# Kernel optimization log

Measured on AMD Instinct MI355X. Metric: run time of the kernel, lower is better.

## Reference

```python
import jax, jax.numpy as jnp
import numpy as np

VOCAB = 21128
D_WENLAN = 2048
SENT_LEN = 44  # hard-coded in original forward


def setup_inputs() -> dict:
    key = jax.random.key(0)
    ks = jax.random.split(key, 8)
    B, S, P = 32, 8, 32
    L = S * SENT_LEN  # 352
    concat_output = jax.random.normal(ks[0], (B, S, D_WENLAN), jnp.float32)
    input_ids = jax.random.randint(ks[1], (B, L), 0, VOCAB, jnp.int32)
    topic_ids = jax.random.randint(ks[2], (B, P), 0, VOCAB, jnp.int32)
    tpw_att_mask = jnp.ones((B, P), jnp.int32)
    tpw_type_ids = jnp.zeros((B, P), jnp.int32)
    attention_mask = jnp.ones((B, L), jnp.int32)
    type_ids = jax.random.randint(ks[3], (B, L), 0, 8, jnp.int32)
    token_table = jax.random.normal(ks[4], (VOCAB, D_WENLAN), jnp.float32) * 0.02
    W1 = jax.random.normal(ks[5], (D_WENLAN, 512), jnp.float32) * 0.02
    b1 = jnp.zeros((512,), jnp.float32)
    W2 = jax.random.normal(ks[6], (512, 768), jnp.float32) * 0.02
    b2 = jnp.zeros((768,), jnp.float32)
    return dict(concat_output=concat_output, input_ids=input_ids, topic_ids=topic_ids,
                tpw_att_mask=tpw_att_mask, tpw_type_ids=tpw_type_ids,
                attention_mask=attention_mask, type_ids=type_ids,
                token_table=token_table, W1=W1, b1=b1, W2=W2, b2=b2)


def reference(concat_output, input_ids, topic_ids, tpw_att_mask, tpw_type_ids,
              attention_mask, type_ids, token_table, W1, b1, W2, b2):
    B, S, D = concat_output.shape
    # vectorized replacement of the python double-loop dict lookups:
    topic_emb = token_table[topic_ids]                      # [B,P,2048]
    inp_emb = token_table[input_ids]                        # [B,L,2048]
    # scatter-add: each sentence block of 44 tokens gets its concat_output row added
    inp_emb = inp_emb.reshape(B, S, SENT_LEN, D) + concat_output[:, :, None, :]
    input_embs = jnp.concatenate([topic_emb, inp_emb.reshape(B, S * SENT_LEN, D)], axis=1)
    # projector MLP (Linear -> tanh -> Linear)
    h = jnp.tanh(jnp.einsum('btd,dk->btk', input_embs, W1) + b1)
    gpt_input_embs = jnp.einsum('btk,ke->bte', h, W2) + b2   # [B,P+L,768]
    # auxiliary concatenated tensors fed to gpt2 (is_train=True path)
    labels = jnp.concatenate([topic_ids, input_ids], axis=1)
    full_type_ids = jnp.concatenate([tpw_type_ids, type_ids], axis=1)
    full_att_mask = jnp.concatenate([tpw_att_mask, attention_mask], axis=1)
    return gpt_input_embs, labels, full_type_ids, full_att_mask
```

## Files before the change

### kernel.cpp

```cpp
#include <hip/hip_runtime.h>
#include <math.h>

typedef _Float16 half8 __attribute__((ext_vector_type(8)));
typedef float f32x4 __attribute__((ext_vector_type(4)));

#define BB 32
#define SS 8
#define PP 32
#define SENT 44
#define LL 352
#define TT 384
#define DD 2048
#define H1 512
#define H2 768
#define MM (BB*TT)
#define OUT0 (MM*H2)

#define GLL16(g, l) __builtin_amdgcn_global_load_lds( \
    (const __attribute__((address_space(1))) void*)(g), \
    (__attribute__((address_space(3))) void*)(l), 16, 0, 0)

__global__ __launch_bounds__(256) void transpose_f16_kernel(
    const float* __restrict__ src, _Float16* __restrict__ dst, int R, int C)
{
    __shared__ float tile[32][33];
    int c0 = blockIdx.x * 32;
    int r0 = blockIdx.y * 32;
    int tx = threadIdx.x & 31;
    int ty = threadIdx.x >> 5;
    #pragma unroll
    for (int i = 0; i < 4; ++i)
        tile[ty + i*8][tx] = src[(size_t)(r0 + ty + i*8) * C + c0 + tx];
    __syncthreads();
    #pragma unroll
    for (int i = 0; i < 4; ++i)
        dst[(size_t)(c0 + ty + i*8) * R + r0 + tx] = (_Float16)tile[tx][ty + i*8];
}

__global__ __launch_bounds__(256) void gemm1_kernel(
    const float*    __restrict__ token_table,
    const int*      __restrict__ topic_ids,
    const int*      __restrict__ input_ids,
    const float*    __restrict__ concat_output,
    const _Float16* __restrict__ W1T,
    const float*    __restrict__ b1,
    _Float16*       __restrict__ Hout)
{
    const int tid  = threadIdx.x;
    const int wid  = tid >> 6;
    const int lane = tid & 63;

    const int logical = ((blockIdx.x & 7) * 48) + (blockIdx.x >> 3);
    const int bm = logical >> 1;
    const int bn = logical & 1;

    __shared__ _Float16 As[2][64 * 64];
    __shared__ _Float16 Bs[2][256 * 64];

    const int arow = tid >> 2;
    const int akq  = (tid & 3) * 16;
    const int aswz = (arow & 7) << 3;

    {
    }
    const int m = bm * 64 + arow;
    const int b = m / TT;
    const int t = m % TT;
    const float* aptr;
    const float* addp = nullptr;
    if (t < PP) {
        aptr = token_table + (size_t)topic_ids[b * PP + t] * DD;
    } else {
        int u = t - PP;
        aptr = token_table + (size_t)input_ids[b * LL + u] * DD;
        addp = concat_output + ((size_t)b * SS + (u / SENT)) * DD;
    }

    const int rl = lane >> 3;
    const int cg = lane & 7;
    const _Float16* bsrc = W1T + (size_t)(bn * 256 + wid * 64 + rl) * DD
                               + ((cg ^ rl) << 3);

    #define G1B(buf, k0) {                                                 \
        _Pragma("unroll")                                                  \
        for (int q = 0; q < 8; ++q)                                        \
            GLL16(bsrc + (size_t)q * 8 * DD + (k0),                        \
                  &Bs[buf][(wid * 8 + q) * 512]);                          \
    }

    #define LOADA(S, k0) {                                                 \
        const float* ap = aptr + (k0) + akq;                               \
        float4 v0 = *(const float4*)(ap);                                  \
        float4 v1 = *(const float4*)(ap + 4);                              \
        float4 v2 = *(const float4*)(ap + 8);                              \
        float4 v3 = *(const float4*)(ap + 12);                             \
        if (addp) {                                                        \
            const float* cp = addp + (k0) + akq;                           \
            float4 c0 = *(const float4*)(cp);                              \
            float4 c1 = *(const float4*)(cp + 4);                          \
            float4 c2 = *(const float4*)(cp + 8);                          \
            float4 c3 = *(const float4*)(cp + 12);                         \
            v0.x += c0.x; v0.y += c0.y; v0.z += c0.z; v0.w += c0.w;        \
            v1.x += c1.x; v1.y += c1.y; v1.z += c1.z; v1.w += c1.w;        \
            v2.x += c2.x; v2.y += c2.y; v2.z += c2.z; v2.w += c2.w;        \
            v3.x += c3.x; v3.y += c3.y; v3.z += c3.z; v3.w += c3.w;        \
        }                                                                  \
        S[0]=v0.x; S[1]=v0.y; S[2]=v0.z; S[3]=v0.w;                        \
        S[4]=v1.x; S[5]=v1.y; S[6]=v1.z; S[7]=v1.w;                        \
        S[8]=v2.x; S[9]=v2.y; S[10]=v2.z; S[11]=v2.w;                      \
        S[12]=v3.x; S[13]=v3.y; S[14]=v3.z; S[15]=v3.w;                    \
    }

    #define WRITEA(S, buf) {                                               \
        half8 h0, h1;                                                      \
        _Pragma("unroll")                                                  \
        for (int j = 0; j < 8; ++j) { h0[j] = (_Float16)S[j];              \
                                      h1[j] = (_Float16)S[8 + j]; }        \
        *(half8*)&As[buf][(arow * 64 + akq) ^ aswz]     = h0;              \
        *(half8*)&As[buf][(arow * 64 + akq + 8) ^ aswz] = h1;              \
    }

    const int wrow = (wid >> 1) * 32;
    const int wcol = (wid & 1) * 128;
    const int fr   = lane & 15;
    const int fg   = lane >> 4;

    f32x4 acc[2][8] = {};

    #define MFMAP(buf) {                                                   \
        _Pragma("unroll")                                                  \
        for (int kk = 0; kk < 2; ++kk) {                                   \
            half8 af[2], bf[8];                                            \
            _Pragma("unroll")                                              \
            for (int i = 0; i < 2; ++i) {                                  \
                int row = wrow + i * 16 + fr;                              \
                af[i] = *(const half8*)&As[buf][                           \
                    (row * 64 + kk * 32 + fg * 8) ^ ((row & 7) << 3)];     \
            }                                                              \
            _Pragma("unroll")                                              \
            for (int j = 0; j < 8; ++j) {                                  \
                int row = wcol + j * 16 + fr;                              \
                bf[j] = *(const half8*)&Bs[buf][                           \
                    (row * 64 + kk * 32 + fg * 8) ^ ((row & 7) << 3)];     \
            }                                                              \
            _Pragma("unroll")                                              \
            for (int i = 0; i < 2; ++i)                                    \
                _Pragma("unroll")                                          \
                for (int j = 0; j < 8; ++j)                                \
                    acc[i][j] = __builtin_amdgcn_mfma_f32_16x16x32_f16(    \
                        af[i], bf[j], acc[i][j], 0, 0, 0);                 \
        }                                                                  \
    }

    float a0[16], a1[16];

    G1B(0, 0);
    LOADA(a0, 0);
    LOADA(a1, 64);
    WRITEA(a0, 0);
    __syncthreads();

    for (int tt = 0; tt < 16; ++tt) {
        const int t2 = tt * 2;
        G1B(1, (t2 + 1) * 64);
        if (t2 + 2 < 32) LOADA(a0, (t2 + 2) * 64);
        MFMAP(0);
        WRITEA(a1, 1);
        __syncthreads();
        if (t2 + 2 < 32) G1B(0, (t2 + 2) * 64);
        if (t2 + 3 < 32) LOADA(a1, (t2 + 3) * 64);
        MFMAP(1);
        if (t2 + 2 < 32) WRITEA(a0, 0);
        __syncthreads();
    }

    #pragma unroll
    for (int i = 0; i < 2; ++i) {
        #pragma unroll
        for (int j = 0; j < 8; ++j) {
            int col = bn * 256 + wcol + j * 16 + fr;
            float bias = b1[col];
            #pragma unroll
            for (int r = 0; r < 4; ++r) {
                int row = bm * 64 + wrow + i * 16 + fg * 4 + r;
                Hout[(size_t)row * H1 + col] = (_Float16)tanhf(acc[i][j][r] + bias);
            }
        }
    }
    #undef G1B
    #undef LOADA
    #undef WRITEA
    #undef MFMAP
}

__global__ __launch_bounds__(256) void gemm2_kernel(
    const _Float16* __restrict__ Hin,
    const _Float16* __restrict__ W2T,
    const float*    __restrict__ b2,
    float*          __restrict__ out)
{
    const int tid  = threadIdx.x;
    const int wid  = tid >> 6;
    const int lane = tid & 63;

    const int logical = ((blockIdx.x & 7) * 72) + (blockIdx.x >> 3);
    const int bm = logical / 6;
    const int bn = logical % 6;

    __shared__ _Float16 As[2][128 * 64];
    __shared__ _Float16 Bs[2][128 * 64];

    const int rl = lane >> 3;
    const int cg = lane & 7;
    const _Float16* asrc = Hin + (size_t)(bm * 128 + wid * 32 + rl) * H1
                               + ((cg ^ rl) << 3);
    const _Float16* bsrc = W2T + (size_t)(bn * 128 + wid * 32 + rl) * H1
                               + ((cg ^ rl) << 3);

    #define G2_ISSUE(buf, k0) {                                            \
        _Pragma("unroll")                                                  \
        for (int q = 0; q < 4; ++q) {                                      \
            GLL16(asrc + (size_t)q * 8 * H1 + (k0),                        \
                  &As[buf][(wid * 4 + q) * 512]);                          \
            GLL16(bsrc + (size_t)q * 8 * H1 + (k0),                        \
                  &Bs[buf][(wid * 4 + q) * 512]);                          \
        }                                                                  \
    }

    const int wrow = (wid >> 1) * 64;
    const int wcol = (wid & 1) * 64;
    const int fr   = lane & 15;
    const int fg   = lane >> 4;

    f32x4 acc[4][4] = {};

    G2_ISSUE(0, 0);

    const int NT = H1 / 64;
    for (int t = 0; t < NT; ++t) {
        __syncthreads();
        if (t + 1 < NT) G2_ISSUE((t + 1) & 1, (t + 1) * 64);
        const int cb = t & 1;
        #pragma unroll
        for (int kk = 0; kk < 2; ++kk) {
            half8 af[4], bf[4];
            #pragma unroll
            for (int i = 0; i < 4; ++i) {
                int row = wrow + i * 16 + fr;
                af[i] = *(const half8*)&As[cb][
                    (row * 64 + kk * 32 + fg * 8) ^ ((row & 7) << 3)];
            }
            #pragma unroll
            for (int j = 0; j < 4; ++j) {
                int row = wcol + j * 16 + fr;
                bf[j] = *(const half8*)&Bs[cb][
                    (row * 64 + kk * 32 + fg * 8) ^ ((row & 7) << 3)];
            }
            #pragma unroll
            for (int i = 0; i < 4; ++i)
                #pragma unroll
                for (int j = 0; j < 4; ++j)
                    acc[i][j] = __builtin_amdgcn_mfma_f32_16x16x32_f16(af[i], bf[j], acc[i][j], 0, 0, 0);
        }
    }

    #pragma unroll
    for (int i = 0; i < 4; ++i) {
        #pragma unroll
        for (int j = 0; j < 4; ++j) {
            int col = bn * 128 + wcol + j * 16 + fr;
            float bias = b2[col];
            #pragma unroll
            for (int r = 0; r < 4; ++r) {
                int row = bm * 128 + wrow + i * 16 + fg * 4 + r;
                out[(size_t)row * H2 + col] = acc[i][j][r] + bias;
            }
        }
    }
    #undef G2_ISSUE
}

__global__ __launch_bounds__(256) void aux_kernel(
    const int* __restrict__ topic_ids,
    const int* __restrict__ input_ids,
    const int* __restrict__ tpw_type_ids,
    const int* __restrict__ type_ids,
    const int* __restrict__ tpw_att_mask,
    const int* __restrict__ attention_mask,
    float* __restrict__ out)
{
    int idx = blockIdx.x * 256 + threadIdx.x;
    if (idx >= MM) return;
    int b = idx / TT, t = idx % TT;
    int lab, ty, mk;
    if (t < PP) {
        lab = topic_ids[b * PP + t];
        ty  = tpw_type_ids[b * PP + t];
        mk  = tpw_att_mask[b * PP + t];
    } else {
        int u = t - PP;
        lab = input_ids[b * LL + u];
        ty  = type_ids[b * LL + u];
        mk  = attention_mask[b * LL + u];
    }
    out[OUT0 + idx]          = (float)lab;
    out[OUT0 + MM + idx]     = (float)ty;
    out[OUT0 + 2 * MM + idx] = (float)mk;
}

extern "C" void kernel_launch(void* const* d_in, const int* in_sizes, int n_in,
                              void* d_out, int out_size, void* d_ws, size_t ws_size,
                              hipStream_t stream) {
    const float* concat_output  = (const float*)d_in[0];
    const int*   input_ids      = (const int*)d_in[1];
    const int*   topic_ids      = (const int*)d_in[2];
    const int*   tpw_att_mask   = (const int*)d_in[3];
    const int*   tpw_type_ids   = (const int*)d_in[4];
    const int*   attention_mask = (const int*)d_in[5];
    const int*   type_ids       = (const int*)d_in[6];
    const float* token_table    = (const float*)d_in[7];
    const float* W1             = (const float*)d_in[8];
    const float* b1             = (const float*)d_in[9];
    const float* W2             = (const float*)d_in[10];
    const float* b2             = (const float*)d_in[11];
    float* out = (float*)d_out;

    _Float16* w1t = (_Float16*)d_ws;
    _Float16* w2t = w1t + (size_t)H1 * DD;
    _Float16* Hws = w2t + (size_t)H2 * H1;

    transpose_f16_kernel<<<dim3(H1 / 32, DD / 32), 256, 0, stream>>>(W1, w1t, DD, H1);
    transpose_f16_kernel<<<dim3(H2 / 32, H1 / 32), 256, 0, stream>>>(W2, w2t, H1, H2);
    aux_kernel<<<(MM + 255) / 256, 256, 0, stream>>>(
        topic_ids, input_ids, tpw_type_ids, type_ids, tpw_att_mask, attention_mask, out);

    gemm1_kernel<<<(MM / 64) * (H1 / 256), 256, 0, stream>>>(
        token_table, topic_ids, input_ids, concat_output, w1t, b1, Hws);
    gemm2_kernel<<<(MM / 128) * (H2 / 128), 256, 0, stream>>>(Hws, w2t, b2, out);
}
```

Baseline: 104.3 us.

## Precompute concat_output projection separately and retile both GEMMs

```diff
diff --git a/kernel.cpp b/kernel.cpp
--- a/kernel.cpp
+++ b/kernel.cpp
@@ -37,160 +37,245 @@
         dst[(size_t)(c0 + ty + i*8) * R + r0 + tx] = (_Float16)tile[tx][ty + i*8];
 }
 
+#define LOADA_T(S, ap, k0) {                                               \
+    const float* _p = (ap) + (k0) + akq;                                   \
+    float4 v0 = *(const float4*)(_p);                                      \
+    float4 v1 = *(const float4*)(_p + 4);                                  \
+    float4 v2 = *(const float4*)(_p + 8);                                  \
+    float4 v3 = *(const float4*)(_p + 12);                                 \
+    S[0]=v0.x; S[1]=v0.y; S[2]=v0.z; S[3]=v0.w;                            \
+    S[4]=v1.x; S[5]=v1.y; S[6]=v1.z; S[7]=v1.w;                            \
+    S[8]=v2.x; S[9]=v2.y; S[10]=v2.z; S[11]=v2.w;                          \
+    S[12]=v3.x; S[13]=v3.y; S[14]=v3.z; S[15]=v3.w;                        \
+}
+
+#define WRITEA_T(S, dst) {                                                 \
+    half8 h0, h1;                                                          \
+    _Pragma("unroll")                                                      \
+    for (int _j = 0; _j < 8; ++_j) { h0[_j] = (_Float16)S[_j];             \
+                                     h1[_j] = (_Float16)S[8 + _j]; }       \
+    *(half8*)&dst[(arow * 64 + akq) ^ aswz]     = h0;                      \
+    *(half8*)&dst[(arow * 64 + akq + 8) ^ aswz] = h1;                      \
+}
+
+__global__ __launch_bounds__(256) void c1_kernel(
+    const float*    __restrict__ concat_output,
+    const _Float16* __restrict__ W1T,
+    float*          __restrict__ C1)
+{
+    const int tid  = threadIdx.x;
+    const int wid  = tid >> 6;
+    const int lane = tid & 63;
+    const int bm = blockIdx.x >> 2;
+    const int bn = blockIdx.x & 3;
+
+    __shared__ _Float16 As[2][64 * 64];
+    __shared__ _Float16 Bs[2][128 * 64];
+
+    const int arow = tid >> 2;
+    const int akq  = (tid & 3) * 16;
+    const int aswz = (arow & 7) << 3;
+    const float* aptr = concat_output + (size_t)(bm * 64 + arow) * DD;
+
+    const int rl = lane >> 3;
+    const int cg = lane & 7;
+    const _Float16* bsrc = W1T + (size_t)(bn * 128 + wid * 32 + rl) * DD
+                               + ((cg ^ rl) << 3);
+
+    #define C1B(buf, k0) {                                                \
+        _Pragma("unroll")                                                 \
+        for (int q = 0; q < 4; ++q)                                       \
+            GLL16(bsrc + (size_t)q * 8 * DD + (k0),                       \
+                  &Bs[buf][(wid * 4 + q) * 512]);                         \
+    }
+
+    const int wrow = (wid >> 1) * 32;
+    const int wcol = (wid & 1) * 64;
+    const int fr   = lane & 15;
+    const int fg   = lane >> 4;
+
+    f32x4 acc[2][4] = {};
+    float a0[16], a1[16];
+
+    C1B(0, 0);
+    LOADA_T(a0, aptr, 0);
+    LOADA_T(a1, aptr, 64);
+    WRITEA_T(a0, As[0]);
+    __syncthreads();
+
+    #define C1_MFMA(buf) {                                                \
+        _Pragma("unroll")                                                 \
+        for (int kk = 0; kk < 2; ++kk) {                                  \
+            half8 af[2], bf[4];                                           \
+            _Pragma("unroll")                                             \
+            for (int i = 0; i < 2; ++i) {                                 \
+                int row = wrow + i * 16 + fr;                             \
+                af[i] = *(const half8*)&As[buf][                          \
+                    (row * 64 + kk * 32 + fg * 8) ^ ((row & 7) << 3)];    \
+            }                                                             \
+            _Pragma("unroll")                                             \
+            for (int j = 0; j < 4; ++j) {                                 \
+                int row = wcol + j * 16 + fr;                             \
+                bf[j] = *(const half8*)&Bs[buf][                          \
+                    (row * 64 + kk * 32 + fg * 8) ^ ((row & 7) << 3)];    \
+            }                                                             \
+            _Pragma("unroll")                                             \
+            for (int i = 0; i < 2; ++i)                                   \
+                _Pragma("unroll")                                         \
+                for (int j = 0; j < 4; ++j)                               \
+                    acc[i][j] = __builtin_amdgcn_mfma_f32_16x16x32_f16(   \
+                        af[i], bf[j], acc[i][j], 0, 0, 0);                \
+        }                                                                 \
+    }
+
+    for (int tt = 0; tt < 16; ++tt) {
+        const int t2 = tt * 2;
+        C1B(1, (t2 + 1) * 64);
+        if (t2 + 2 < 32) LOADA_T(a0, aptr, (t2 + 2) * 64);
+        C1_MFMA(0);
+        WRITEA_T(a1, As[1]);
+        __syncthreads();
+        if (t2 + 2 < 32) C1B(0, (t2 + 2) * 64);
+        if (t2 + 3 < 32) LOADA_T(a1, aptr, (t2 + 3) * 64);
+        C1_MFMA(1);
+        if (t2 + 2 < 32) WRITEA_T(a0, As[0]);
+        __syncthreads();
+    }
+
+    #pragma unroll
+    for (int i = 0; i < 2; ++i)
+        #pragma unroll
+        for (int j = 0; j < 4; ++j) {
+            int col = bn * 128 + wcol + j * 16 + fr;
+            #pragma unroll
+            for (int r = 0; r < 4; ++r) {
+                int row = bm * 64 + wrow + i * 16 + fg * 4 + r;
+                C1[(size_t)row * H1 + col] = acc[i][j][r];
+            }
+        }
+    #undef C1B
+    #undef C1_MFMA
+}
+
 __global__ __launch_bounds__(256) void gemm1_kernel(
     const float*    __restrict__ token_table,
     const int*      __restrict__ topic_ids,
     const int*      __restrict__ input_ids,
-    const float*    __restrict__ concat_output,
     const _Float16* __restrict__ W1T,
     const float*    __restrict__ b1,
+    const float*    __restrict__ C1,
     _Float16*       __restrict__ Hout)
 {
     const int tid  = threadIdx.x;
     const int wid  = tid >> 6;
     const int lane = tid & 63;
 
-    const int logical = ((blockIdx.x & 7) * 48) + (blockIdx.x >> 3);
-    const int bm = logical >> 1;
-    const int bn = logical & 1;
+    const int logical = ((blockIdx.x & 7) * 96) + (blockIdx.x >> 3);
+    const int bm = logical >> 2;
+    const int bn = logical & 3;
 
     __shared__ _Float16 As[2][64 * 64];
-    __shared__ _Float16 Bs[2][256 * 64];
+    __shared__ _Float16 Bs[2][128 * 64];
 
     const int arow = tid >> 2;
     const int akq  = (tid & 3) * 16;
     const int aswz = (arow & 7) << 3;
 
-    {
-    }
     const int m = bm * 64 + arow;
     const int b = m / TT;
     const int t = m % TT;
     const float* aptr;
-    const float* addp = nullptr;
     if (t < PP) {
         aptr = token_table + (size_t)topic_ids[b * PP + t] * DD;
     } else {
-        int u = t - PP;
-        aptr = token_table + (size_t)input_ids[b * LL + u] * DD;
-        addp = concat_output + ((size_t)b * SS + (u / SENT)) * DD;
+        aptr = token_table + (size_t)input_ids[b * LL + (t - PP)] * DD;
     }
 
     const int rl = lane >> 3;
     const int cg = lane & 7;
-    const _Float16* bsrc = W1T + (size_t)(bn * 256 + wid * 64 + rl) * DD
+    const _Float16* bsrc = W1T + (size_t)(bn * 128 + wid * 32 + rl) * DD
                                + ((cg ^ rl) << 3);
 
-    #define G1B(buf, k0) {                                                 \
-        _Pragma("unroll")                                                  \
-        for (int q = 0; q < 8; ++q)                                        \
-            GLL16(bsrc + (size_t)q * 8 * DD + (k0),                        \
-                  &Bs[buf][(wid * 8 + q) * 512]);                          \
-    }
-
-    #define LOADA(S, k0) {                                                 \
-        const float* ap = aptr + (k0) + akq;                               \
-        float4 v0 = *(const float4*)(ap);                                  \
-        float4 v1 = *(const float4*)(ap + 4);                              \
-        float4 v2 = *(const float4*)(ap + 8);                              \
-        float4 v3 = *(const float4*)(ap + 12);                             \
-        if (addp) {                                                        \
-            const float* cp = addp + (k0) + akq;                           \
-            float4 c0 = *(const float4*)(cp);                              \
-            float4 c1 = *(const float4*)(cp + 4);                          \
-            float4 c2 = *(const float4*)(cp + 8);                          \
-            float4 c3 = *(const float4*)(cp + 12);                         \
-            v0.x += c0.x; v0.y += c0.y; v0.z += c0.z; v0.w += c0.w;        \
-            v1.x += c1.x; v1.y += c1.y; v1.z += c1.z; v1.w += c1.w;        \
-            v2.x += c2.x; v2.y += c2.y; v2.z += c2.z; v2.w += c2.w;        \
-            v3.x += c3.x; v3.y += c3.y; v3.z += c3.z; v3.w += c3.w;        \
-        }                                                                  \
-        S[0]=v0.x; S[1]=v0.y; S[2]=v0.z; S[3]=v0.w;                        \
-        S[4]=v1.x; S[5]=v1.y; S[6]=v1.z; S[7]=v1.w;                        \
-        S[8]=v2.x; S[9]=v2.y; S[10]=v2.z; S[11]=v2.w;                      \
-        S[12]=v3.x; S[13]=v3.y; S[14]=v3.z; S[15]=v3.w;                    \
-    }
-
-    #define WRITEA(S, buf) {                                               \
-        half8 h0, h1;                                                      \
-        _Pragma("unroll")                                                  \
-        for (int j = 0; j < 8; ++j) { h0[j] = (_Float16)S[j];              \
-                                      h1[j] = (_Float16)S[8 + j]; }        \
-        *(half8*)&As[buf][(arow * 64 + akq) ^ aswz]     = h0;              \
-        *(half8*)&As[buf][(arow * 64 + akq + 8) ^ aswz] = h1;              \
+    #define G1B(buf, k0) {                                                \
+        _Pragma("unroll")                                                 \
+        for (int q = 0; q < 4; ++q)                                       \
+            GLL16(bsrc + (size_t)q * 8 * DD + (k0),                       \
+                  &Bs[buf][(wid * 4 + q) * 512]);                         \
     }
 
     const int wrow = (wid >> 1) * 32;
-    const int wcol = (wid & 1) * 128;
+    const int wcol = (wid & 1) * 64;
     const int fr   = lane & 15;
     const int fg   = lane >> 4;
 
-    f32x4 acc[2][8] = {};
-
-    #define MFMAP(buf) {                                                   \
-        _Pragma("unroll")                                                  \
-        for (int kk = 0; kk < 2; ++kk) {                                   \
-            half8 af[2], bf[8];                                            \
-            _Pragma("unroll")                                              \
-            for (int i = 0; i < 2; ++i) {                                  \
-                int row = wrow + i * 16 + fr;                              \
-                af[i] = *(const half8*)&As[buf][                           \
-                    (row * 64 + kk * 32 + fg * 8) ^ ((row & 7) << 3)];     \
-            }                                                              \
-            _Pragma("unroll")                                              \
-            for (int j = 0; j < 8; ++j) {                                  \
-                int row = wcol + j * 16 + fr;                              \
-                bf[j] = *(const half8*)&Bs[buf][                           \
-                    (row * 64 + kk * 32 + fg * 8) ^ ((row & 7) << 3)];     \
-            }                                                              \
-            _Pragma("unroll")                                              \
-            for (int i = 0; i < 2; ++i)                                    \
-                _Pragma("unroll")                                          \
-                for (int j = 0; j < 8; ++j)                                \
-                    acc[i][j] = __builtin_amdgcn_mfma_f32_16x16x32_f16(    \
-                        af[i], bf[j], acc[i][j], 0, 0, 0);                 \
-        }                                                                  \
-    }
-
+    f32x4 acc[2][4] = {};
     float a0[16], a1[16];
 
     G1B(0, 0);
-    LOADA(a0, 0);
-    LOADA(a1, 64);
-    WRITEA(a0, 0);
+    LOADA_T(a0, aptr, 0);
+    LOADA_T(a1, aptr, 64);
+    WRITEA_T(a0, As[0]);
     __syncthreads();
+
+    #define G1_MFMA(buf) {                                                \
+        _Pragma("unroll")                                                 \
+        for (int kk = 0; kk < 2; ++kk) {                                  \
+            half8 af[2], bf[4];                                           \
+            _Pragma("unroll")                                             \
+            for (int i = 0; i < 2; ++i) {                                 \
+                int row = wrow + i * 16 + fr;                             \
+                af[i] = *(const half8*)&As[buf][                          \
+                    (row * 64 + kk * 32 + fg * 8) ^ ((row & 7) << 3)];    \
+            }                                                             \
+            _Pragma("unroll")                                             \
+            for (int j = 0; j < 4; ++j) {                                 \
+                int row = wcol + j * 16 + fr;                             \
+                bf[j] = *(const half8*)&Bs[buf][                          \
+                    (row * 64 + kk * 32 + fg * 8) ^ ((row & 7) << 3)];    \
+            }                                                             \
+            _Pragma("unroll")                                             \
+            for (int i = 0; i < 2; ++i)                                   \
+                _Pragma("unroll")                                         \
+                for (int j = 0; j < 4; ++j)                               \
+                    acc[i][j] = __builtin_amdgcn_mfma_f32_16x16x32_f16(   \
+                        af[i], bf[j], acc[i][j], 0, 0, 0);                \
+        }                                                                 \
+    }
 
     for (int tt = 0; tt < 16; ++tt) {
         const int t2 = tt * 2;
         G1B(1, (t2 + 1) * 64);
-        if (t2 + 2 < 32) LOADA(a0, (t2 + 2) * 64);
-        MFMAP(0);
-        WRITEA(a1, 1);
+        if (t2 + 2 < 32) LOADA_T(a0, aptr, (t2 + 2) * 64);
+        G1_MFMA(0);
+        WRITEA_T(a1, As[1]);
         __syncthreads();
         if (t2 + 2 < 32) G1B(0, (t2 + 2) * 64);
-        if (t2 + 3 < 32) LOADA(a1, (t2 + 3) * 64);
-        MFMAP(1);
-        if (t2 + 2 < 32) WRITEA(a0, 0);
+        if (t2 + 3 < 32) LOADA_T(a1, aptr, (t2 + 3) * 64);
+        G1_MFMA(1);
+        if (t2 + 2 < 32) WRITEA_T(a0, As[0]);
         __syncthreads();
     }
 
     #pragma unroll
     for (int i = 0; i < 2; ++i) {
         #pragma unroll
-        for (int j = 0; j < 8; ++j) {
-            int col = bn * 256 + wcol + j * 16 + fr;
+        for (int j = 0; j < 4; ++j) {
+            int col = bn * 128 + wcol + j * 16 + fr;
             float bias = b1[col];
             #pragma unroll
             for (int r = 0; r < 4; ++r) {
                 int row = bm * 64 + wrow + i * 16 + fg * 4 + r;
-                Hout[(size_t)row * H1 + col] = (_Float16)tanhf(acc[i][j][r] + bias);
+                int rb = row / TT;
+                int rt = row - rb * TT;
+                float v = acc[i][j][r] + bias;
+                if (rt >= PP)
+                    v += C1[(size_t)(rb * SS + (rt - PP) / SENT) * H1 + col];
+                Hout[(size_t)row * H1 + col] = (_Float16)tanhf(v);
             }
         }
     }
     #undef G1B
-    #undef LOADA
-    #undef WRITEA
-    #undef MFMAP
+    #undef G1_MFMA
 }
 
 __global__ __launch_bounds__(256) void gemm2_kernel(
@@ -203,36 +288,37 @@
     const int wid  = tid >> 6;
     const int lane = tid & 63;
 
-    const int logical = ((blockIdx.x & 7) * 72) + (blockIdx.x >> 3);
-    const int bm = logical / 6;
-    const int bn = logical % 6;
-
-    __shared__ _Float16 As[2][128 * 64];
-    __shared__ _Float16 Bs[2][128 * 64];
+    const int logical = ((blockIdx.x & 7) * 64) + (blockIdx.x >> 3);
+    const int bm = logical >> 2;
+    const int bn = logical & 3;
+
+    __shared__ _Float16 As[2][96 * 64];
+    __shared__ _Float16 Bs[2][192 * 64];
 
     const int rl = lane >> 3;
     const int cg = lane & 7;
-    const _Float16* asrc = Hin + (size_t)(bm * 128 + wid * 32 + rl) * H1
+    const _Float16* asrc = Hin + (size_t)(bm * 96 + wid * 24 + rl) * H1
                                + ((cg ^ rl) << 3);
-    const _Float16* bsrc = W2T + (size_t)(bn * 128 + wid * 32 + rl) * H1
+    const _Float16* bsrc = W2T + (size_t)(bn * 192 + wid * 48 + rl) * H1
                                + ((cg ^ rl) << 3);
 
-    #define G2_ISSUE(buf, k0) {                                            \
-        _Pragma("unroll")                                                  \
-        for (int q = 0; q < 4; ++q) {                                      \
-            GLL16(asrc + (size_t)q * 8 * H1 + (k0),                        \
-                  &As[buf][(wid * 4 + q) * 512]);                          \
-            GLL16(bsrc + (size_t)q * 8 * H1 + (k0),                        \
-                  &Bs[buf][(wid * 4 + q) * 512]);                          \
-        }                                                                  \
-    }
-
-    const int wrow = (wid >> 1) * 64;
-    const int wcol = (wid & 1) * 64;
+    #define G2_ISSUE(buf, k0) {                                           \
+        _Pragma("unroll")                                                 \
+        for (int q = 0; q < 3; ++q)                                       \
+            GLL16(asrc + (size_t)q * 8 * H1 + (k0),                       \
+                  &As[buf][(wid * 3 + q) * 512]);                         \
+        _Pragma("unroll")                                                 \
+        for (int q = 0; q < 6; ++q)                                       \
+            GLL16(bsrc + (size_t)q * 8 * H1 + (k0),                       \
+                  &Bs[buf][(wid * 6 + q) * 512]);                         \
+    }
+
+    const int wrow = (wid >> 1) * 48;
+    const int wcol = (wid & 1) * 96;
     const int fr   = lane & 15;
     const int fg   = lane >> 4;
 
-    f32x4 acc[4][4] = {};
+    f32x4 acc[3][6] = {};
 
     G2_ISSUE(0, 0);
 
@@ -243,36 +329,36 @@
         const int cb = t & 1;
         #pragma unroll
         for (int kk = 0; kk < 2; ++kk) {
-            half8 af[4], bf[4];
-            #pragma unroll
-            for (int i = 0; i < 4; ++i) {
+            half8 af[3], bf[6];
+            #pragma unroll
+            for (int i = 0; i < 3; ++i) {
                 int row = wrow + i * 16 + fr;
                 af[i] = *(const half8*)&As[cb][
                     (row * 64 + kk * 32 + fg * 8) ^ ((row & 7) << 3)];
             }
             #pragma unroll
-            for (int j = 0; j < 4; ++j) {
+            for (int j = 0; j < 6; ++j) {
                 int row = wcol + j * 16 + fr;
                 bf[j] = *(const half8*)&Bs[cb][
                     (row * 64 + kk * 32 + fg * 8) ^ ((row & 7) << 3)];
             }
             #pragma unroll
-            for (int i = 0; i < 4; ++i)
+            for (int i = 0; i < 3; ++i)
                 #pragma unroll
-                for (int j = 0; j < 4; ++j)
+                for (int j = 0; j < 6; ++j)
                     acc[i][j] = __builtin_amdgcn_mfma_f32_16x16x32_f16(af[i], bf[j], acc[i][j], 0, 0, 0);
         }
     }
 
     #pragma unroll
-    for (int i = 0; i < 4; ++i) {
+    for (int i = 0; i < 3; ++i) {
         #pragma unroll
-        for (int j = 0; j < 4; ++j) {
-            int col = bn * 128 + wcol + j * 16 + fr;
+        for (int j = 0; j < 6; ++j) {
+            int col = bn * 192 + wcol + j * 16 + fr;
             float bias = b2[col];
             #pragma unroll
             for (int r = 0; r < 4; ++r) {
-                int row = bm * 128 + wrow + i * 16 + fg * 4 + r;
+                int row = bm * 96 + wrow + i * 16 + fg * 4 + r;
                 out[(size_t)row * H2 + col] = acc[i][j][r] + bias;
             }
         }
@@ -328,13 +414,15 @@
     _Float16* w1t = (_Float16*)d_ws;
     _Float16* w2t = w1t + (size_t)H1 * DD;
     _Float16* Hws = w2t + (size_t)H2 * H1;
+    float*    C1w = (float*)(Hws + (size_t)MM * H1);
 
     transpose_f16_kernel<<<dim3(H1 / 32, DD / 32), 256, 0, stream>>>(W1, w1t, DD, H1);
     transpose_f16_kernel<<<dim3(H2 / 32, H1 / 32), 256, 0, stream>>>(W2, w2t, H1, H2);
     aux_kernel<<<(MM + 255) / 256, 256, 0, stream>>>(
         topic_ids, input_ids, tpw_type_ids, type_ids, tpw_att_mask, attention_mask, out);
-
-    gemm1_kernel<<<(MM / 64) * (H1 / 256), 256, 0, stream>>>(
-        token_table, topic_ids, input_ids, concat_output, w1t, b1, Hws);
-    gemm2_kernel<<<(MM / 128) * (H2 / 128), 256, 0, stream>>>(Hws, w2t, b2, out);
-}
+    c1_kernel<<<16, 256, 0, stream>>>(concat_output, w1t, C1w);
+
+    gemm1_kernel<<<(MM / 64) * (H1 / 128), 256, 0, stream>>>(
+        token_table, topic_ids, input_ids, w1t, b1, C1w, Hws);
+    gemm2_kernel<<<(MM / 96) * (H2 / 192), 256, 0, stream>>>(Hws, w2t, b2, out);
+}
```

New measurement: 110.4 us. +5.9%, slower.
